# Kernel tuning notes

Hardware: AMD Instinct MI355X
Metric: run time of the kernel (lower is better)

## Reference

```python
import jax, jax.numpy as jnp
import numpy as np

TEMPERATURE = 1.0
NEG = -1e9
EPS = 1e-8


def setup_inputs() -> dict:
    key = jax.random.key(0)
    k1, k2, k3 = jax.random.split(key, 3)
    B, H = 524288, 32
    scores = jax.random.normal(k1, (B, H), dtype=jnp.float32)
    rankings = jax.random.randint(k2, (B, H), 0, 33, dtype=jnp.int32)
    mask = jax.random.randint(k3, (B, H), 0, 2, dtype=jnp.int32).astype(bool)
    return {"scores": scores, "rankings": rankings, "mask": mask}


def reference(scores, rankings, mask):
    B, H = scores.shape
    # effective validity: horse present AND has a ranking > 0 (top_k=None)
    m = mask & (rankings > 0)
    # masked, temperature-scaled scores; -1e9 entries underflow to exactly 0 in softmax
    s = jnp.where(m, scores / TEMPERATURE, NEG)
    p = jax.nn.softmax(s, axis=1)  # [B, H], ~0 at invalid slots

    n_valid = jnp.sum(m, axis=1)  # [B]
    # ideal order: valid horses sorted by ranking ascending (invalid pushed to end)
    rank_key = jnp.where(m, rankings, jnp.iinfo(jnp.int32).max)
    rank_order = jnp.argsort(rank_key, axis=1)          # stable sort
    # prediction order: valid horses in original index order (matches torch.where)
    pos_order = jnp.argsort(~m, axis=1)                 # stable: valid first

    q = jnp.take_along_axis(p, rank_order, axis=1)      # ideal_probs, aligned by list position
    pr = jnp.take_along_axis(p, pos_order, axis=1)      # pred_probs,  aligned by list position

    # positions >= n_valid are padding
    valid_pos = jnp.arange(H)[None, :] < n_valid[:, None]
    q_safe = jnp.where(valid_pos, q, 1.0)
    pr_safe = jnp.where(valid_pos, pr, 1.0)
    # KL(ideal || pred) with the original's log(pred + 1e-8)
    kl_terms = q_safe * (jnp.log(q_safe) - jnp.log(pr_safe + EPS))
    kl = jnp.sum(jnp.where(valid_pos, kl_terms, 0.0), axis=1)  # [B]

    # rows with <= 1 valid ranked horse are skipped entirely
    row_ok = n_valid > 1
    n_rows = jnp.maximum(jnp.sum(row_ok), 1)
    return jnp.sum(jnp.where(row_ok, kl, 0.0)) / n_rows  # reduction='mean'
```

## Files before the change

### kernel.cpp

```cpp
#include <hip/hip_runtime.h>
#include <stdint.h>


#define H 32
#define BLK 256
#define WPB 4
#define ROWD 17
#define WREGION (64 * ROWD)

typedef short s16x2 __attribute__((ext_vector_type(2)));
union PK { uint32_t u; s16x2 v; };

__global__ __launch_bounds__(BLK) void listwise_kernel(
    const float* __restrict__ scores,
    const int* __restrict__ rankings,
    const unsigned char* __restrict__ mask_u8,
    float* __restrict__ part_kl,
    float* __restrict__ part_cnt,
    int nrows)
{
    __shared__ uint32_t stage[WPB * WREGION];
    __shared__ float s_kl[WPB], s_cnt[WPB];

    const int tid  = threadIdx.x;
    const int lane = tid & 63;
    const int wid  = tid >> 6;
    uint32_t* wbuf = &stage[wid * WREGION];
    const int wrow0 = blockIdx.x * BLK + wid * 64;

    unsigned char probe = mask_u8[lane];
    const bool mask_is_i32 =
        (__ballot(((lane & 3) != 0) && (probe != 0)) == 0ull);

    float kl = 0.0f, cnt = 0.0f;

    uint32_t kp[16], sp[16];
    int nv = 0;
    bool have_row = false;
    unsigned short* rowp = (unsigned short*)&wbuf[lane * ROWD];

    if (wrow0 + 64 <= nrows) {
        have_row = true;

        const uint4* r4 = (const uint4*)(rankings + (size_t)wrow0 * H);
        if (mask_is_i32) {
            const uint4* m4 =
                (const uint4*)((const uint32_t*)mask_u8 + (size_t)wrow0 * H);
            #pragma unroll
            for (int c = 0; c < 8; ++c) {
                const uint4 rv = r4[lane + 64 * c];
                const uint4 mv = m4[lane + 64 * c];
                const int L = (lane + 64 * c) << 2;
                const uint32_t t0 = (mv.x != 0u && (int)rv.x > 0) ? (rv.x << 5) : 0x4000u;
                const uint32_t t1 = (mv.y != 0u && (int)rv.y > 0) ? (rv.y << 5) : 0x4000u;
                const uint32_t t2 = (mv.z != 0u && (int)rv.z > 0) ? (rv.z << 5) : 0x4000u;
                const uint32_t t3 = (mv.w != 0u && (int)rv.w > 0) ? (rv.w << 5) : 0x4000u;
                uint32_t* d = &wbuf[(L >> 5) * ROWD + ((L & 31) >> 1)];
                d[0] = t0 | (t1 << 16);
                d[1] = t2 | (t3 << 16);
            }
        } else {
            const uint32_t* m1 = (const uint32_t*)(mask_u8 + (size_t)wrow0 * H);
            #pragma unroll
            for (int c = 0; c < 8; ++c) {
                const uint4 rv = r4[lane + 64 * c];
                const uint32_t mv = m1[lane + 64 * c];
                const int L = (lane + 64 * c) << 2;
                const uint32_t t0 = ((mv & 0x000000FFu) != 0u && (int)rv.x > 0) ? (rv.x << 5) : 0x4000u;
                const uint32_t t1 = ((mv & 0x0000FF00u) != 0u && (int)rv.y > 0) ? (rv.y << 5) : 0x4000u;
                const uint32_t t2 = ((mv & 0x00FF0000u) != 0u && (int)rv.z > 0) ? (rv.z << 5) : 0x4000u;
                const uint32_t t3 = ((mv & 0xFF000000u) != 0u && (int)rv.w > 0) ? (rv.w << 5) : 0x4000u;
                uint32_t* d = &wbuf[(L >> 5) * ROWD + ((L & 31) >> 1)];
                d[0] = t0 | (t1 << 16);
                d[1] = t2 | (t3 << 16);
            }
        }
        {
            const uint32_t* rb = &wbuf[lane * ROWD];
            uint32_t inv2 = 0;
            #pragma unroll
            for (int a = 0; a < 16; ++a) {
                const uint32_t w = rb[a];
                kp[a] = w | ((uint32_t)(2 * a) | (((uint32_t)(2 * a + 1)) << 16));
                inv2 += (w >> 14) & 0x00010001u;
            }
            nv = 32 - (int)((inv2 & 0xFFFFu) + (inv2 >> 16));
        }

        {
            const uint4* g4 = (const uint4*)(scores + (size_t)wrow0 * H);
            #pragma unroll
            for (int c = 0; c < 8; ++c) {
                const uint4 v = g4[lane + 64 * c];
                const int L = (lane + 64 * c) << 2;
                const uint32_t b0 = (v.x + 0x8000u) >> 16;
                const uint32_t b1 = (v.y + 0x8000u) >> 16;
                const uint32_t b2 = (v.z + 0x8000u) >> 16;
                const uint32_t b3 = (v.w + 0x8000u) >> 16;
                uint32_t* d = &wbuf[(L >> 5) * ROWD + ((L & 31) >> 1)];
                d[0] = b0 | (b1 << 16);
                d[1] = b2 | (b3 << 16);
            }
            const uint32_t* rb = &wbuf[lane * ROWD];
            int jp = 0;
            #pragma unroll
            for (int a = 0; a < 16; ++a) {
                const uint32_t sw = rb[a];
                sp[a] = sw;
                const uint32_t kw = kp[a];
                const bool v0 = (kw & 0xFFFFu) < 0x4000u;
                const bool v1 = (kw >> 16) < 0x4000u;
                rowp[v0 ? jp : 33] = (unsigned short)(sw & 0xFFFFu);
                jp += v0 ? 1 : 0;
                rowp[v1 ? jp : 33] = (unsigned short)(sw >> 16);
                jp += v1 ? 1 : 0;
            }
        }
    } else if (wrow0 + lane < nrows) {
        have_row = true;
        const int row = wrow0 + lane;
        const int*   rptr = rankings + (size_t)row * H;
        const float* sptr = scores + (size_t)row * H;
        uint32_t vbits = 0;
        if (mask_is_i32) {
            const int* mp = (const int*)mask_u8 + (size_t)row * H;
            #pragma unroll
            for (int k = 0; k < H; ++k) vbits |= (mp[k] != 0 ? 1u : 0u) << k;
        } else {
            const unsigned char* mp = mask_u8 + (size_t)row * H;
            #pragma unroll
            for (int k = 0; k < H; ++k) vbits |= (mp[k] != 0 ? 1u : 0u) << k;
        }
        int jp = 0;
        #pragma unroll
        for (int a = 0; a < 16; ++a) {
            uint32_t kq[2], bq[2];
            #pragma unroll
            for (int q = 0; q < 2; ++q) {
                const int k = 2 * a + q;
                const int r = rptr[k];
                const bool valid = (((vbits >> k) & 1u) != 0u) && (r > 0);
                kq[q] = valid ? ((((uint32_t)r) << 5) | (uint32_t)k)
                              : (0x4000u | (uint32_t)k);
                nv += valid ? 1 : 0;
                bq[q] = (__float_as_uint(sptr[k]) + 0x8000u) >> 16;
                rowp[valid ? jp : 33] = (unsigned short)bq[q];
                jp += valid ? 1 : 0;
            }
            kp[a] = kq[0] | (kq[1] << 16);
            sp[a] = bq[0] | (bq[1] << 16);
        }
    }

    if (have_row) {
        float se = 0.0f, num = 0.0f;
        #pragma unroll
        for (int i = 0; i < H; ++i) {
            const uint32_t pw = kp[i / 2];
            const uint32_t k16 = (i & 1) ? (pw >> 16) : (pw & 0xFFFFu);
            PK b; b.u = (k16 << 16) | k16;
            PK acc; acc.u = 0;
            #pragma unroll
            for (int m = 0; m < 16; ++m) {
                PK pm; pm.u = kp[m];
                s16x2 d = pm.v - b.v;
                acc.v = acc.v - (d >> 15);
            }
            const int j = (int)acc.v.x + (int)acc.v.y;
            const float g = __uint_as_float(((uint32_t)rowp[j]) << 16);
            const uint32_t sw = sp[i / 2];
            const float s_i = __uint_as_float((i & 1) ? (sw & 0xFFFF0000u)
                                                      : (sw << 16));
            const bool valid = k16 < 0x4000u;
            float e = __expf(s_i);
            e = valid ? e : 0.0f;
            const float d2 = valid ? (s_i - g) : 0.0f;
            se += e;
            num = __builtin_fmaf(e, d2, num);
        }
        if (nv > 1) { kl = __fdividef(num, se); cnt = 1.0f; }
    }

    #pragma unroll
    for (int m = 32; m >= 1; m >>= 1) {
        kl  += __shfl_xor(kl, m);
        cnt += __shfl_xor(cnt, m);
    }
    if (lane == 0) { s_kl[wid] = kl; s_cnt[wid] = cnt; }
    __syncthreads();
    if (tid == 0) {
        part_kl[blockIdx.x]  = s_kl[0] + s_kl[1] + s_kl[2] + s_kl[3];
        part_cnt[blockIdx.x] = s_cnt[0] + s_cnt[1] + s_cnt[2] + s_cnt[3];
    }
}

__global__ __launch_bounds__(256) void finalize_kernel(
    const float* __restrict__ part_kl,
    const float* __restrict__ part_cnt,
    float* __restrict__ out, int nblk)
{
    float k = 0.0f, c = 0.0f;
    for (int i = threadIdx.x; i < nblk; i += 256) {
        k += part_kl[i];
        c += part_cnt[i];
    }
    #pragma unroll
    for (int m = 32; m >= 1; m >>= 1) {
        k += __shfl_xor(k, m);
        c += __shfl_xor(c, m);
    }
    __shared__ float sk[4], sc[4];
    const int wid = threadIdx.x >> 6;
    if ((threadIdx.x & 63) == 0) { sk[wid] = k; sc[wid] = c; }
    __syncthreads();
    if (threadIdx.x == 0) {
        float K = sk[0] + sk[1] + sk[2] + sk[3];
        float C = sc[0] + sc[1] + sc[2] + sc[3];
        if (C < 1.0f) C = 1.0f;
        out[0] = K / C;
    }
}

extern "C" void kernel_launch(void* const* d_in, const int* in_sizes, int n_in,
                              void* d_out, int out_size, void* d_ws, size_t ws_size,
                              hipStream_t stream) {
    const float* scores = (const float*)d_in[0];
    const int* rankings = (const int*)d_in[1];
    const unsigned char* mask = (const unsigned char*)d_in[2];
    float* out = (float*)d_out;

    const int total = in_sizes[0];
    const int nrows = total / H;
    const int blocks = (nrows + BLK - 1) / BLK;

    float* part_kl  = (float*)d_ws;
    float* part_cnt = (float*)d_ws + blocks;

    listwise_kernel<<<blocks, BLK, 0, stream>>>(
        scores, rankings, mask, part_kl, part_cnt, nrows);

    finalize_kernel<<<1, 256, 0, stream>>>(part_kl, part_cnt, out, blocks);
}
```

Before: 207.2 us.

## Process two 64-row tiles per wave with register prefetch of next tile

Each wave now handles two 64-row tiles. Rankings, scores and the byte mask for the first tile are loaded into registers up front, and the next tile's loads are issued while the current tile is staged through LDS, so memory latency overlaps with compute. The grid shrinks by half and launch bounds request 4 blocks per SIMD. This costs extra VGPRs for the prefetch buffers, which could cause spills or lower occupancy.

```diff
diff --git a/kernel.cpp b/kernel.cpp
--- a/kernel.cpp
+++ b/kernel.cpp
@@ -5,13 +5,14 @@
 #define H 32
 #define BLK 256
 #define WPB 4
+#define NT 2
 #define ROWD 17
 #define WREGION (64 * ROWD)
 
 typedef short s16x2 __attribute__((ext_vector_type(2)));
 union PK { uint32_t u; s16x2 v; };
 
-__global__ __launch_bounds__(BLK) void listwise_kernel(
+__global__ __launch_bounds__(BLK, 4) void listwise_kernel(
     const float* __restrict__ scores,
     const int* __restrict__ rankings,
     const unsigned char* __restrict__ mask_u8,
@@ -26,72 +27,105 @@
     const int lane = tid & 63;
     const int wid  = tid >> 6;
     uint32_t* wbuf = &stage[wid * WREGION];
-    const int wrow0 = blockIdx.x * BLK + wid * 64;
+    const int wave_g   = blockIdx.x * WPB + wid;
+    const int row_base = wave_g * (NT * 64);
+
+    uint4 pr[8], ps[8];
+    uint32_t pmw[8];
+    const bool t0_full = (row_base + 64 <= nrows);
+    if (t0_full) {
+        const uint4* r4 = (const uint4*)(rankings + (size_t)row_base * H);
+        const uint4* s4 = (const uint4*)(scores + (size_t)row_base * H);
+        #pragma unroll
+        for (int c = 0; c < 8; ++c) pr[c] = r4[lane + 64 * c];
+        #pragma unroll
+        for (int c = 0; c < 8; ++c) ps[c] = s4[lane + 64 * c];
+    }
 
     unsigned char probe = mask_u8[lane];
     const bool mask_is_i32 =
         (__ballot(((lane & 3) != 0) && (probe != 0)) == 0ull);
+    if (t0_full && !mask_is_i32) {
+        const uint32_t* m1 = (const uint32_t*)(mask_u8 + (size_t)row_base * H);
+        #pragma unroll
+        for (int c = 0; c < 8; ++c) pmw[c] = m1[lane + 64 * c];
+    }
 
     float kl = 0.0f, cnt = 0.0f;
-
-    uint32_t kp[16], sp[16];
-    int nv = 0;
-    bool have_row = false;
     unsigned short* rowp = (unsigned short*)&wbuf[lane * ROWD];
 
-    if (wrow0 + 64 <= nrows) {
-        have_row = true;
-
-        const uint4* r4 = (const uint4*)(rankings + (size_t)wrow0 * H);
-        if (mask_is_i32) {
-            const uint4* m4 =
-                (const uint4*)((const uint32_t*)mask_u8 + (size_t)wrow0 * H);
+    #pragma unroll
+    for (int t = 0; t < NT; ++t) {
+        const int wrow0 = row_base + t * 64;
+        uint32_t kp[16], sp[16];
+        int nv = 0;
+        bool have = false;
+
+        if (wrow0 + 64 <= nrows) {
+            have = true;
+
+            if (!mask_is_i32) {
+                #pragma unroll
+                for (int c = 0; c < 8; ++c) {
+                    const uint4 rv = pr[c];
+                    const uint32_t mv = pmw[c];
+                    const int L = (lane + 64 * c) << 2;
+                    const uint32_t t0 = ((mv & 0x000000FFu) != 0u && (int)rv.x > 0) ? (rv.x << 5) : 0x4000u;
+                    const uint32_t t1 = ((mv & 0x0000FF00u) != 0u && (int)rv.y > 0) ? (rv.y << 5) : 0x4000u;
+                    const uint32_t t2 = ((mv & 0x00FF0000u) != 0u && (int)rv.z > 0) ? (rv.z << 5) : 0x4000u;
+                    const uint32_t t3 = ((mv & 0xFF000000u) != 0u && (int)rv.w > 0) ? (rv.w << 5) : 0x4000u;
+                    uint32_t* d = &wbuf[(L >> 5) * ROWD + ((L & 31) >> 1)];
+                    d[0] = t0 | (t1 << 16);
+                    d[1] = t2 | (t3 << 16);
+                }
+            } else {
+                const uint4* m4 =
+                    (const uint4*)((const uint32_t*)mask_u8 + (size_t)wrow0 * H);
+                #pragma unroll
+                for (int c = 0; c < 8; ++c) {
+                    const uint4 rv = pr[c];
+                    const uint4 mv = m4[lane + 64 * c];
+                    const int L = (lane + 64 * c) << 2;
+                    const uint32_t t0 = (mv.x != 0u && (int)rv.x > 0) ? (rv.x << 5) : 0x4000u;
+                    const uint32_t t1 = (mv.y != 0u && (int)rv.y > 0) ? (rv.y << 5) : 0x4000u;
+                    const uint32_t t2 = (mv.z != 0u && (int)rv.z > 0) ? (rv.z << 5) : 0x4000u;
+                    const uint32_t t3 = (mv.w != 0u && (int)rv.w > 0) ? (rv.w << 5) : 0x4000u;
+                    uint32_t* d = &wbuf[(L >> 5) * ROWD + ((L & 31) >> 1)];
+                    d[0] = t0 | (t1 << 16);
+                    d[1] = t2 | (t3 << 16);
+                }
+            }
+
+            if (t + 1 < NT) {
+                const int nr0 = row_base + (t + 1) * 64;
+                if (nr0 + 64 <= nrows) {
+                    const uint4* r4n = (const uint4*)(rankings + (size_t)nr0 * H);
+                    #pragma unroll
+                    for (int c = 0; c < 8; ++c) pr[c] = r4n[lane + 64 * c];
+                    if (!mask_is_i32) {
+                        const uint32_t* m1n =
+                            (const uint32_t*)(mask_u8 + (size_t)nr0 * H);
+                        #pragma unroll
+                        for (int c = 0; c < 8; ++c) pmw[c] = m1n[lane + 64 * c];
+                    }
+                }
+            }
+
+            {
+                const uint32_t* rb = &wbuf[lane * ROWD];
+                uint32_t inv2 = 0;
+                #pragma unroll
+                for (int a = 0; a < 16; ++a) {
+                    const uint32_t w = rb[a];
+                    kp[a] = w | ((uint32_t)(2 * a) | (((uint32_t)(2 * a + 1)) << 16));
+                    inv2 += (w >> 14) & 0x00010001u;
+                }
+                nv = 32 - (int)((inv2 & 0xFFFFu) + (inv2 >> 16));
+            }
+
             #pragma unroll
             for (int c = 0; c < 8; ++c) {
-                const uint4 rv = r4[lane + 64 * c];
-                const uint4 mv = m4[lane + 64 * c];
-                const int L = (lane + 64 * c) << 2;
-                const uint32_t t0 = (mv.x != 0u && (int)rv.x > 0) ? (rv.x << 5) : 0x4000u;
-                const uint32_t t1 = (mv.y != 0u && (int)rv.y > 0) ? (rv.y << 5) : 0x4000u;
-                const uint32_t t2 = (mv.z != 0u && (int)rv.z > 0) ? (rv.z << 5) : 0x4000u;
-                const uint32_t t3 = (mv.w != 0u && (int)rv.w > 0) ? (rv.w << 5) : 0x4000u;
-                uint32_t* d = &wbuf[(L >> 5) * ROWD + ((L & 31) >> 1)];
-                d[0] = t0 | (t1 << 16);
-                d[1] = t2 | (t3 << 16);
-            }
-        } else {
-            const uint32_t* m1 = (const uint32_t*)(mask_u8 + (size_t)wrow0 * H);
-            #pragma unroll
-            for (int c = 0; c < 8; ++c) {
-                const uint4 rv = r4[lane + 64 * c];
-                const uint32_t mv = m1[lane + 64 * c];
-                const int L = (lane + 64 * c) << 2;
-                const uint32_t t0 = ((mv & 0x000000FFu) != 0u && (int)rv.x > 0) ? (rv.x << 5) : 0x4000u;
-                const uint32_t t1 = ((mv & 0x0000FF00u) != 0u && (int)rv.y > 0) ? (rv.y << 5) : 0x4000u;
-                const uint32_t t2 = ((mv & 0x00FF0000u) != 0u && (int)rv.z > 0) ? (rv.z << 5) : 0x4000u;
-                const uint32_t t3 = ((mv & 0xFF000000u) != 0u && (int)rv.w > 0) ? (rv.w << 5) : 0x4000u;
-                uint32_t* d = &wbuf[(L >> 5) * ROWD + ((L & 31) >> 1)];
-                d[0] = t0 | (t1 << 16);
-                d[1] = t2 | (t3 << 16);
-            }
-        }
-        {
-            const uint32_t* rb = &wbuf[lane * ROWD];
-            uint32_t inv2 = 0;
-            #pragma unroll
-            for (int a = 0; a < 16; ++a) {
-                const uint32_t w = rb[a];
-                kp[a] = w | ((uint32_t)(2 * a) | (((uint32_t)(2 * a + 1)) << 16));
-                inv2 += (w >> 14) & 0x00010001u;
-            }
-            nv = 32 - (int)((inv2 & 0xFFFFu) + (inv2 >> 16));
-        }
-
-        {
-            const uint4* g4 = (const uint4*)(scores + (size_t)wrow0 * H);
-            #pragma unroll
-            for (int c = 0; c < 8; ++c) {
-                const uint4 v = g4[lane + 64 * c];
+                const uint4 v = ps[c];
                 const int L = (lane + 64 * c) << 2;
                 const uint32_t b0 = (v.x + 0x8000u) >> 16;
                 const uint32_t b1 = (v.y + 0x8000u) >> 16;
@@ -101,84 +135,96 @@
                 d[0] = b0 | (b1 << 16);
                 d[1] = b2 | (b3 << 16);
             }
-            const uint32_t* rb = &wbuf[lane * ROWD];
+
+            if (t + 1 < NT) {
+                const int nr0 = row_base + (t + 1) * 64;
+                if (nr0 + 64 <= nrows) {
+                    const uint4* s4n = (const uint4*)(scores + (size_t)nr0 * H);
+                    #pragma unroll
+                    for (int c = 0; c < 8; ++c) ps[c] = s4n[lane + 64 * c];
+                }
+            }
+
+            {
+                const uint32_t* rb = &wbuf[lane * ROWD];
+                int jp = 0;
+                #pragma unroll
+                for (int a = 0; a < 16; ++a) {
+                    const uint32_t sw = rb[a];
+                    sp[a] = sw;
+                    const uint32_t kw = kp[a];
+                    const bool v0 = (kw & 0xFFFFu) < 0x4000u;
+                    const bool v1 = (kw >> 16) < 0x4000u;
+                    rowp[v0 ? jp : 33] = (unsigned short)(sw & 0xFFFFu);
+                    jp += v0 ? 1 : 0;
+                    rowp[v1 ? jp : 33] = (unsigned short)(sw >> 16);
+                    jp += v1 ? 1 : 0;
+                }
+            }
+        } else if (wrow0 + lane < nrows) {
+            have = true;
+            const int row = wrow0 + lane;
+            const int*   rptr = rankings + (size_t)row * H;
+            const float* sptr = scores + (size_t)row * H;
+            uint32_t vbits = 0;
+            if (mask_is_i32) {
+                const int* mp = (const int*)mask_u8 + (size_t)row * H;
+                #pragma unroll
+                for (int k = 0; k < H; ++k) vbits |= (mp[k] != 0 ? 1u : 0u) << k;
+            } else {
+                const unsigned char* mp = mask_u8 + (size_t)row * H;
+                #pragma unroll
+                for (int k = 0; k < H; ++k) vbits |= (mp[k] != 0 ? 1u : 0u) << k;
+            }
             int jp = 0;
             #pragma unroll
             for (int a = 0; a < 16; ++a) {
-                const uint32_t sw = rb[a];
-                sp[a] = sw;
-                const uint32_t kw = kp[a];
-                const bool v0 = (kw & 0xFFFFu) < 0x4000u;
-                const bool v1 = (kw >> 16) < 0x4000u;
-                rowp[v0 ? jp : 33] = (unsigned short)(sw & 0xFFFFu);
-                jp += v0 ? 1 : 0;
-                rowp[v1 ? jp : 33] = (unsigned short)(sw >> 16);
-                jp += v1 ? 1 : 0;
+                uint32_t kq[2], bq[2];
+                #pragma unroll
+                for (int q = 0; q < 2; ++q) {
+                    const int k = 2 * a + q;
+                    const int r = rptr[k];
+                    const bool valid = (((vbits >> k) & 1u) != 0u) && (r > 0);
+                    kq[q] = valid ? ((((uint32_t)r) << 5) | (uint32_t)k)
+                                  : (0x4000u | (uint32_t)k);
+                    nv += valid ? 1 : 0;
+                    bq[q] = (__float_as_uint(sptr[k]) + 0x8000u) >> 16;
+                    rowp[valid ? jp : 33] = (unsigned short)bq[q];
+                    jp += valid ? 1 : 0;
+                }
+                kp[a] = kq[0] | (kq[1] << 16);
+                sp[a] = bq[0] | (bq[1] << 16);
             }
         }
-    } else if (wrow0 + lane < nrows) {
-        have_row = true;
-        const int row = wrow0 + lane;
-        const int*   rptr = rankings + (size_t)row * H;
-        const float* sptr = scores + (size_t)row * H;
-        uint32_t vbits = 0;
-        if (mask_is_i32) {
-            const int* mp = (const int*)mask_u8 + (size_t)row * H;
+
+        if (have) {
+            float se = 0.0f, num = 0.0f;
             #pragma unroll
-            for (int k = 0; k < H; ++k) vbits |= (mp[k] != 0 ? 1u : 0u) << k;
-        } else {
-            const unsigned char* mp = mask_u8 + (size_t)row * H;
-            #pragma unroll
-            for (int k = 0; k < H; ++k) vbits |= (mp[k] != 0 ? 1u : 0u) << k;
+            for (int i = 0; i < H; ++i) {
+                const uint32_t pw = kp[i / 2];
+                const uint32_t k16 = (i & 1) ? (pw >> 16) : (pw & 0xFFFFu);
+                PK b; b.u = (k16 << 16) | k16;
+                PK acc; acc.u = 0;
+                #pragma unroll
+                for (int m = 0; m < 16; ++m) {
+                    PK pm_; pm_.u = kp[m];
+                    s16x2 d = pm_.v - b.v;
+                    acc.v = acc.v - (d >> 15);
+                }
+                const int j = (int)acc.v.x + (int)acc.v.y;
+                const float g = __uint_as_float(((uint32_t)rowp[j]) << 16);
+                const uint32_t sw = sp[i / 2];
+                const float s_i = __uint_as_float((i & 1) ? (sw & 0xFFFF0000u)
+                                                          : (sw << 16));
+                const bool valid = k16 < 0x4000u;
+                float e = __expf(s_i);
+                e = valid ? e : 0.0f;
+                const float d2 = valid ? (s_i - g) : 0.0f;
+                se += e;
+                num = __builtin_fmaf(e, d2, num);
+            }
+            if (nv > 1) { kl += __fdividef(num, se); cnt += 1.0f; }
         }
-        int jp = 0;
-        #pragma unroll
-        for (int a = 0; a < 16; ++a) {
-            uint32_t kq[2], bq[2];
-            #pragma unroll
-            for (int q = 0; q < 2; ++q) {
-                const int k = 2 * a + q;
-                const int r = rptr[k];
-                const bool valid = (((vbits >> k) & 1u) != 0u) && (r > 0);
-                kq[q] = valid ? ((((uint32_t)r) << 5) | (uint32_t)k)
-                              : (0x4000u | (uint32_t)k);
-                nv += valid ? 1 : 0;
-                bq[q] = (__float_as_uint(sptr[k]) + 0x8000u) >> 16;
-                rowp[valid ? jp : 33] = (unsigned short)bq[q];
-                jp += valid ? 1 : 0;
-            }
-            kp[a] = kq[0] | (kq[1] << 16);
-            sp[a] = bq[0] | (bq[1] << 16);
-        }
-    }
-
-    if (have_row) {
-        float se = 0.0f, num = 0.0f;
-        #pragma unroll
-        for (int i = 0; i < H; ++i) {
-            const uint32_t pw = kp[i / 2];
-            const uint32_t k16 = (i & 1) ? (pw >> 16) : (pw & 0xFFFFu);
-            PK b; b.u = (k16 << 16) | k16;
-            PK acc; acc.u = 0;
-            #pragma unroll
-            for (int m = 0; m < 16; ++m) {
-                PK pm; pm.u = kp[m];
-                s16x2 d = pm.v - b.v;
-                acc.v = acc.v - (d >> 15);
-            }
-            const int j = (int)acc.v.x + (int)acc.v.y;
-            const float g = __uint_as_float(((uint32_t)rowp[j]) << 16);
-            const uint32_t sw = sp[i / 2];
-            const float s_i = __uint_as_float((i & 1) ? (sw & 0xFFFF0000u)
-                                                      : (sw << 16));
-            const bool valid = k16 < 0x4000u;
-            float e = __expf(s_i);
-            e = valid ? e : 0.0f;
-            const float d2 = valid ? (s_i - g) : 0.0f;
-            se += e;
-            num = __builtin_fmaf(e, d2, num);
-        }
-        if (nv > 1) { kl = __fdividef(num, se); cnt = 1.0f; }
     }
 
     #pragma unroll
@@ -231,7 +277,8 @@
 
     const int total = in_sizes[0];
     const int nrows = total / H;
-    const int blocks = (nrows + BLK - 1) / BLK;
+    const int rows_per_block = WPB * NT * 64;
+    const int blocks = (nrows + rows_per_block - 1) / rows_per_block;
 
     float* part_kl  = (float*)d_ws;
     float* part_cnt = (float*)d_ws + blocks;
```

Measured after the change: 227.8 us. 10.0% more time.

## Replace per-element rank counting with bitonic sort and batch global loads upfront

Applied to the files above, without the earlier changes.

The O(H^2) packed-int16 rank computation is replaced by a 32-element register bitonic sort of (key, score) words. Each slot's score is then paired with the compacted score at the same position read from LDS. All rankings, scores and mask loads for full tiles are also issued before any LDS work so memory latency overlaps. The sort costs roughly 240 compare-exchanges per row and raises register pressure from the 8x uint4 prefetch buffers, which may lower occupancy.

```diff
diff --git a/kernel.cpp b/kernel.cpp
--- a/kernel.cpp
+++ b/kernel.cpp
@@ -7,9 +7,6 @@
 #define WPB 4
 #define ROWD 17
 #define WREGION (64 * ROWD)
-
-typedef short s16x2 __attribute__((ext_vector_type(2)));
-union PK { uint32_t u; s16x2 v; };
 
 __global__ __launch_bounds__(BLK) void listwise_kernel(
     const float* __restrict__ scores,
@@ -28,27 +25,69 @@
     uint32_t* wbuf = &stage[wid * WREGION];
     const int wrow0 = blockIdx.x * BLK + wid * 64;
 
+    float kl = 0.0f, cnt = 0.0f;
+    uint32_t kp[16], sw[16];
+    int nv = 0;
+    bool have_row = false;
+    unsigned short* rowp = (unsigned short*)&wbuf[lane * ROWD];
+
+    const bool full = (wrow0 + 64 <= nrows);
+
+    uint4 pr[8], ps[8];
+    uint32_t pmw[8];
+    if (full) {
+        const uint4* r4 = (const uint4*)(rankings + (size_t)wrow0 * H);
+        const uint4* s4 = (const uint4*)(scores + (size_t)wrow0 * H);
+        const uint32_t* m1 = (const uint32_t*)(mask_u8 + (size_t)wrow0 * H);
+        #pragma unroll
+        for (int c = 0; c < 8; ++c) pr[c] = r4[lane + 64 * c];
+        #pragma unroll
+        for (int c = 0; c < 8; ++c) ps[c] = s4[lane + 64 * c];
+        #pragma unroll
+        for (int c = 0; c < 8; ++c) pmw[c] = m1[lane + 64 * c];
+    }
+
     unsigned char probe = mask_u8[lane];
     const bool mask_is_i32 =
         (__ballot(((lane & 3) != 0) && (probe != 0)) == 0ull);
 
-    float kl = 0.0f, cnt = 0.0f;
-
-    uint32_t kp[16], sp[16];
-    int nv = 0;
-    bool have_row = false;
-    unsigned short* rowp = (unsigned short*)&wbuf[lane * ROWD];
-
-    if (wrow0 + 64 <= nrows) {
+    if (full) {
         have_row = true;
 
-        const uint4* r4 = (const uint4*)(rankings + (size_t)wrow0 * H);
-        if (mask_is_i32) {
+        #pragma unroll
+        for (int c = 0; c < 8; ++c) {
+            const uint4 v = ps[c];
+            const int L = (lane + 64 * c) << 2;
+            uint32_t* d = &wbuf[(L >> 5) * ROWD + ((L & 31) >> 1)];
+            d[0] = ((v.x + 0x8000u) >> 16) | (((v.y + 0x8000u) >> 16) << 16);
+            d[1] = ((v.z + 0x8000u) >> 16) | (((v.w + 0x8000u) >> 16) << 16);
+        }
+        {
+            const uint32_t* rb = &wbuf[lane * ROWD];
+            #pragma unroll
+            for (int a = 0; a < 16; ++a) sw[a] = rb[a];
+        }
+
+        if (!mask_is_i32) {
+            #pragma unroll
+            for (int c = 0; c < 8; ++c) {
+                const uint4 rv = pr[c];
+                const uint32_t mv = pmw[c];
+                const int L = (lane + 64 * c) << 2;
+                const uint32_t t0 = ((mv & 0x000000FFu) != 0u && (int)rv.x > 0) ? (rv.x << 5) : 0x4000u;
+                const uint32_t t1 = ((mv & 0x0000FF00u) != 0u && (int)rv.y > 0) ? (rv.y << 5) : 0x4000u;
+                const uint32_t t2 = ((mv & 0x00FF0000u) != 0u && (int)rv.z > 0) ? (rv.z << 5) : 0x4000u;
+                const uint32_t t3 = ((mv & 0xFF000000u) != 0u && (int)rv.w > 0) ? (rv.w << 5) : 0x4000u;
+                uint32_t* d = &wbuf[(L >> 5) * ROWD + ((L & 31) >> 1)];
+                d[0] = t0 | (t1 << 16);
+                d[1] = t2 | (t3 << 16);
+            }
+        } else {
             const uint4* m4 =
                 (const uint4*)((const uint32_t*)mask_u8 + (size_t)wrow0 * H);
             #pragma unroll
             for (int c = 0; c < 8; ++c) {
-                const uint4 rv = r4[lane + 64 * c];
+                const uint4 rv = pr[c];
                 const uint4 mv = m4[lane + 64 * c];
                 const int L = (lane + 64 * c) << 2;
                 const uint32_t t0 = (mv.x != 0u && (int)rv.x > 0) ? (rv.x << 5) : 0x4000u;
@@ -59,21 +98,6 @@
                 d[0] = t0 | (t1 << 16);
                 d[1] = t2 | (t3 << 16);
             }
-        } else {
-            const uint32_t* m1 = (const uint32_t*)(mask_u8 + (size_t)wrow0 * H);
-            #pragma unroll
-            for (int c = 0; c < 8; ++c) {
-                const uint4 rv = r4[lane + 64 * c];
-                const uint32_t mv = m1[lane + 64 * c];
-                const int L = (lane + 64 * c) << 2;
-                const uint32_t t0 = ((mv & 0x000000FFu) != 0u && (int)rv.x > 0) ? (rv.x << 5) : 0x4000u;
-                const uint32_t t1 = ((mv & 0x0000FF00u) != 0u && (int)rv.y > 0) ? (rv.y << 5) : 0x4000u;
-                const uint32_t t2 = ((mv & 0x00FF0000u) != 0u && (int)rv.z > 0) ? (rv.z << 5) : 0x4000u;
-                const uint32_t t3 = ((mv & 0xFF000000u) != 0u && (int)rv.w > 0) ? (rv.w << 5) : 0x4000u;
-                uint32_t* d = &wbuf[(L >> 5) * ROWD + ((L & 31) >> 1)];
-                d[0] = t0 | (t1 << 16);
-                d[1] = t2 | (t3 << 16);
-            }
         }
         {
             const uint32_t* rb = &wbuf[lane * ROWD];
@@ -86,33 +110,17 @@
             }
             nv = 32 - (int)((inv2 & 0xFFFFu) + (inv2 >> 16));
         }
-
         {
-            const uint4* g4 = (const uint4*)(scores + (size_t)wrow0 * H);
-            #pragma unroll
-            for (int c = 0; c < 8; ++c) {
-                const uint4 v = g4[lane + 64 * c];
-                const int L = (lane + 64 * c) << 2;
-                const uint32_t b0 = (v.x + 0x8000u) >> 16;
-                const uint32_t b1 = (v.y + 0x8000u) >> 16;
-                const uint32_t b2 = (v.z + 0x8000u) >> 16;
-                const uint32_t b3 = (v.w + 0x8000u) >> 16;
-                uint32_t* d = &wbuf[(L >> 5) * ROWD + ((L & 31) >> 1)];
-                d[0] = b0 | (b1 << 16);
-                d[1] = b2 | (b3 << 16);
-            }
-            const uint32_t* rb = &wbuf[lane * ROWD];
             int jp = 0;
             #pragma unroll
             for (int a = 0; a < 16; ++a) {
-                const uint32_t sw = rb[a];
-                sp[a] = sw;
+                const uint32_t s2 = sw[a];
                 const uint32_t kw = kp[a];
                 const bool v0 = (kw & 0xFFFFu) < 0x4000u;
                 const bool v1 = (kw >> 16) < 0x4000u;
-                rowp[v0 ? jp : 33] = (unsigned short)(sw & 0xFFFFu);
+                rowp[v0 ? jp : 33] = (unsigned short)(s2 & 0xFFFFu);
                 jp += v0 ? 1 : 0;
-                rowp[v1 ? jp : 33] = (unsigned short)(sw >> 16);
+                rowp[v1 ? jp : 33] = (unsigned short)(s2 >> 16);
                 jp += v1 ? 1 : 0;
             }
         }
@@ -148,35 +156,55 @@
                 jp += valid ? 1 : 0;
             }
             kp[a] = kq[0] | (kq[1] << 16);
-            sp[a] = bq[0] | (bq[1] << 16);
+            sw[a] = bq[0] | (bq[1] << 16);
         }
     }
 
     if (have_row) {
+        uint32_t w32[32];
+        #pragma unroll
+        for (int a = 0; a < 16; ++a) {
+            const uint32_t kw = kp[a], s2 = sw[a];
+            w32[2 * a]     = (kw << 16) | (s2 & 0xFFFFu);
+            w32[2 * a + 1] = (kw & 0xFFFF0000u) | (s2 >> 16);
+        }
+        #pragma unroll
+        for (int k = 2; k <= 32; k <<= 1) {
+            #pragma unroll
+            for (int j = k >> 1; j > 0; j >>= 1) {
+                #pragma unroll
+                for (int i = 0; i < 32; ++i) {
+                    const int l = i ^ j;
+                    if (l > i) {
+                        const uint32_t a = w32[i], b = w32[l];
+                        const uint32_t mn = a < b ? a : b;
+                        const uint32_t mx = a < b ? b : a;
+                        const bool up = ((i & k) == 0);
+                        w32[i] = up ? mn : mx;
+                        w32[l] = up ? mx : mn;
+                    }
+                }
+            }
+        }
+
         float se = 0.0f, num = 0.0f;
-        #pragma unroll
-        for (int i = 0; i < H; ++i) {
-            const uint32_t pw = kp[i / 2];
-            const uint32_t k16 = (i & 1) ? (pw >> 16) : (pw & 0xFFFFu);
-            PK b; b.u = (k16 << 16) | k16;
-            PK acc; acc.u = 0;
-            #pragma unroll
-            for (int m = 0; m < 16; ++m) {
-                PK pm; pm.u = kp[m];
-                s16x2 d = pm.v - b.v;
-                acc.v = acc.v - (d >> 15);
-            }
-            const int j = (int)acc.v.x + (int)acc.v.y;
-            const float g = __uint_as_float(((uint32_t)rowp[j]) << 16);
-            const uint32_t sw = sp[i / 2];
-            const float s_i = __uint_as_float((i & 1) ? (sw & 0xFFFF0000u)
-                                                      : (sw << 16));
-            const bool valid = k16 < 0x4000u;
-            float e = __expf(s_i);
-            e = valid ? e : 0.0f;
-            const float d2 = valid ? (s_i - g) : 0.0f;
-            se += e;
-            num = __builtin_fmaf(e, d2, num);
+        const uint32_t* rbd = &wbuf[lane * ROWD];
+        #pragma unroll
+        for (int a = 0; a < 16; ++a) {
+            const uint32_t cw = rbd[a];
+            #pragma unroll
+            for (int q = 0; q < 2; ++q) {
+                const uint32_t wv = w32[2 * a + q];
+                const bool valid = wv < 0x40000000u;
+                const float s_i = __uint_as_float(wv << 16);
+                const uint32_t c16 = q ? (cw >> 16) : (cw & 0xFFFFu);
+                const float g = __uint_as_float(c16 << 16);
+                float e = __expf(s_i);
+                e = valid ? e : 0.0f;
+                const float d2 = valid ? (s_i - g) : 0.0f;
+                se += e;
+                num = __builtin_fmaf(e, d2, num);
+            }
         }
         if (nv > 1) { kl = __fdividef(num, se); cnt = 1.0f; }
     }
```

Measured after the change: 199.7 us. 3.6% less time.

## Map rows to lanes with wave-level bitonic sort and ballot compaction

Applied to the files above, without the earlier changes.

Replaces the per-thread row processing, which used LDS staging and quadratic rank counting, with a scheme where each wave handles two rows per step and each lane holds one element. Ranking order comes from a shuffle-based bitonic sort, and valid scores are compacted with ballot/mbcnt plus ds_permute. The softmax-weighted KL terms are then reduced with cross-lane shuffles. The grid becomes a fixed 2048 blocks that loop over row pairs, prefetching the next pair into registers. This drops the LDS traffic and O(H^2) compute, at the cost of narrow 4-byte loads and a serial per-wave loop.

```diff
diff --git a/kernel.cpp b/kernel.cpp
--- a/kernel.cpp
+++ b/kernel.cpp
@@ -5,11 +5,6 @@
 #define H 32
 #define BLK 256
 #define WPB 4
-#define ROWD 17
-#define WREGION (64 * ROWD)
-
-typedef short s16x2 __attribute__((ext_vector_type(2)));
-union PK { uint32_t u; s16x2 v; };
 
 __global__ __launch_bounds__(BLK) void listwise_kernel(
     const float* __restrict__ scores,
@@ -17,176 +12,103 @@
     const unsigned char* __restrict__ mask_u8,
     float* __restrict__ part_kl,
     float* __restrict__ part_cnt,
-    int nrows)
+    int nrows, int ipw)
 {
-    __shared__ uint32_t stage[WPB * WREGION];
     __shared__ float s_kl[WPB], s_cnt[WPB];
 
     const int tid  = threadIdx.x;
     const int lane = tid & 63;
     const int wid  = tid >> 6;
-    uint32_t* wbuf = &stage[wid * WREGION];
-    const int wrow0 = blockIdx.x * BLK + wid * 64;
+    const int e5   = lane & 31;
+    const int h    = lane >> 5;
+
+    const long long wave_g = (long long)blockIdx.x * WPB + wid;
+    const long long tpairs = ((long long)nrows + 1) >> 1;
+    const long long pbase  = wave_g * ipw;
+    const long long pend   = (pbase + ipw < tpairs) ? (pbase + ipw) : tpairs;
 
     unsigned char probe = mask_u8[lane];
     const bool mask_is_i32 =
         (__ballot(((lane & 3) != 0) && (probe != 0)) == 0ull);
 
-    float kl = 0.0f, cnt = 0.0f;
+    float kl_acc = 0.0f, cnt_acc = 0.0f;
 
-    uint32_t kp[16], sp[16];
-    int nv = 0;
-    bool have_row = false;
-    unsigned short* rowp = (unsigned short*)&wbuf[lane * ROWD];
+    if (pbase < pend) {
+        const size_t maxidx = (size_t)nrows * H - 1;
 
-    if (wrow0 + 64 <= nrows) {
-        have_row = true;
+        size_t b = (size_t)pbase * 64 + lane;
+        if (b > maxidx) b = maxidx;
+        int      rv = rankings[b];
+        float    sv = scores[b];
+        uint32_t mv = mask_is_i32 ? (uint32_t)((const int*)mask_u8)[b]
+                                  : (uint32_t)mask_u8[b];
 
-        const uint4* r4 = (const uint4*)(rankings + (size_t)wrow0 * H);
-        if (mask_is_i32) {
-            const uint4* m4 =
-                (const uint4*)((const uint32_t*)mask_u8 + (size_t)wrow0 * H);
+        for (long long p = pbase; p < pend; ++p) {
+            const long long pn = (p + 1 < pend) ? (p + 1) : p;
+            size_t bn = (size_t)pn * 64 + lane;
+            if (bn > maxidx) bn = maxidx;
+            const int      rvn = rankings[bn];
+            const float    svn = scores[bn];
+            const uint32_t mvn = mask_is_i32
+                ? (uint32_t)((const int*)mask_u8)[bn]
+                : (uint32_t)mask_u8[bn];
+
+            const int  row   = (int)(2 * p) + h;
+            const bool valid = (row < nrows) && (mv != 0u) && (rv > 0);
+            const uint32_t b16 = (__float_as_uint(sv) + 0x8000u) >> 16;
+            const uint32_t key = valid ? (((uint32_t)rv << 5) | (uint32_t)e5)
+                                       : (0x4000u | (uint32_t)e5);
+            uint32_t w = (key << 16) | b16;
+            const float gsrc = __uint_as_float(b16 << 16);
+
+            const unsigned long long vm = __ballot(valid);
+            const uint32_t mb = __builtin_amdgcn_mbcnt_hi(
+                (uint32_t)(vm >> 32),
+                __builtin_amdgcn_mbcnt_lo((uint32_t)vm, 0u));
+            const int plo = __builtin_popcountll(vm & 0xffffffffull);
+            const int phi = __builtin_popcountll(vm >> 32);
+            const int q   = (int)mb - (h ? plo : 0);
+            const int nvh = h ? phi : plo;
+            const int slot = (valid ? q : (nvh + (e5 - q))) + (h << 5);
+            const float gq = __uint_as_float(
+                __builtin_amdgcn_ds_permute(slot << 2, (int)__float_as_uint(gsrc)));
+
             #pragma unroll
-            for (int c = 0; c < 8; ++c) {
-                const uint4 rv = r4[lane + 64 * c];
-                const uint4 mv = m4[lane + 64 * c];
-                const int L = (lane + 64 * c) << 2;
-                const uint32_t t0 = (mv.x != 0u && (int)rv.x > 0) ? (rv.x << 5) : 0x4000u;
-                const uint32_t t1 = (mv.y != 0u && (int)rv.y > 0) ? (rv.y << 5) : 0x4000u;
-                const uint32_t t2 = (mv.z != 0u && (int)rv.z > 0) ? (rv.z << 5) : 0x4000u;
-                const uint32_t t3 = (mv.w != 0u && (int)rv.w > 0) ? (rv.w << 5) : 0x4000u;
-                uint32_t* d = &wbuf[(L >> 5) * ROWD + ((L & 31) >> 1)];
-                d[0] = t0 | (t1 << 16);
-                d[1] = t2 | (t3 << 16);
+            for (int k = 2; k <= 32; k <<= 1) {
+                #pragma unroll
+                for (int j = k >> 1; j > 0; j >>= 1) {
+                    const uint32_t pw = (uint32_t)__shfl_xor((int)w, j);
+                    const uint32_t mn = w < pw ? w : pw;
+                    const uint32_t mx = w < pw ? pw : w;
+                    const bool tm = (((e5 & j) == 0) != ((e5 & k) == 0));
+                    w = tm ? mx : mn;
+                }
             }
-        } else {
-            const uint32_t* m1 = (const uint32_t*)(mask_u8 + (size_t)wrow0 * H);
+
+            const bool  vld = (w < 0x40000000u);
+            const float sb  = __uint_as_float(w << 16);
+            float e = __expf(sb);
+            e = vld ? e : 0.0f;
+            const float d = vld ? (sb - gq) : 0.0f;
+            float se = e;
+            float nm = e * d;
             #pragma unroll
-            for (int c = 0; c < 8; ++c) {
-                const uint4 rv = r4[lane + 64 * c];
-                const uint32_t mv = m1[lane + 64 * c];
-                const int L = (lane + 64 * c) << 2;
-                const uint32_t t0 = ((mv & 0x000000FFu) != 0u && (int)rv.x > 0) ? (rv.x << 5) : 0x4000u;
-                const uint32_t t1 = ((mv & 0x0000FF00u) != 0u && (int)rv.y > 0) ? (rv.y << 5) : 0x4000u;
-                const uint32_t t2 = ((mv & 0x00FF0000u) != 0u && (int)rv.z > 0) ? (rv.z << 5) : 0x4000u;
-                const uint32_t t3 = ((mv & 0xFF000000u) != 0u && (int)rv.w > 0) ? (rv.w << 5) : 0x4000u;
-                uint32_t* d = &wbuf[(L >> 5) * ROWD + ((L & 31) >> 1)];
-                d[0] = t0 | (t1 << 16);
-                d[1] = t2 | (t3 << 16);
+            for (int j2 = 1; j2 <= 16; j2 <<= 1) {
+                se += __shfl_xor(se, j2);
+                nm += __shfl_xor(nm, j2);
             }
-        }
-        {
-            const uint32_t* rb = &wbuf[lane * ROWD];
-            uint32_t inv2 = 0;
-            #pragma unroll
-            for (int a = 0; a < 16; ++a) {
-                const uint32_t w = rb[a];
-                kp[a] = w | ((uint32_t)(2 * a) | (((uint32_t)(2 * a + 1)) << 16));
-                inv2 += (w >> 14) & 0x00010001u;
-            }
-            nv = 32 - (int)((inv2 & 0xFFFFu) + (inv2 >> 16));
-        }
+            const bool rok = (nvh > 1);
+            const float contrib = rok ? __fdividef(nm, se) : 0.0f;
+            kl_acc  += (e5 == 0) ? contrib : 0.0f;
+            cnt_acc += (e5 == 0 && rok) ? 1.0f : 0.0f;
 
-        {
-            const uint4* g4 = (const uint4*)(scores + (size_t)wrow0 * H);
-            #pragma unroll
-            for (int c = 0; c < 8; ++c) {
-                const uint4 v = g4[lane + 64 * c];
-                const int L = (lane + 64 * c) << 2;
-                const uint32_t b0 = (v.x + 0x8000u) >> 16;
-                const uint32_t b1 = (v.y + 0x8000u) >> 16;
-                const uint32_t b2 = (v.z + 0x8000u) >> 16;
-                const uint32_t b3 = (v.w + 0x8000u) >> 16;
-                uint32_t* d = &wbuf[(L >> 5) * ROWD + ((L & 31) >> 1)];
-                d[0] = b0 | (b1 << 16);
-                d[1] = b2 | (b3 << 16);
-            }
-            const uint32_t* rb = &wbuf[lane * ROWD];
-            int jp = 0;
-            #pragma unroll
-            for (int a = 0; a < 16; ++a) {
-                const uint32_t sw = rb[a];
-                sp[a] = sw;
-                const uint32_t kw = kp[a];
-                const bool v0 = (kw & 0xFFFFu) < 0x4000u;
-                const bool v1 = (kw >> 16) < 0x4000u;
-                rowp[v0 ? jp : 33] = (unsigned short)(sw & 0xFFFFu);
-                jp += v0 ? 1 : 0;
-                rowp[v1 ? jp : 33] = (unsigned short)(sw >> 16);
-                jp += v1 ? 1 : 0;
-            }
-        }
-    } else if (wrow0 + lane < nrows) {
-        have_row = true;
-        const int row = wrow0 + lane;
-        const int*   rptr = rankings + (size_t)row * H;
-        const float* sptr = scores + (size_t)row * H;
-        uint32_t vbits = 0;
-        if (mask_is_i32) {
-            const int* mp = (const int*)mask_u8 + (size_t)row * H;
-            #pragma unroll
-            for (int k = 0; k < H; ++k) vbits |= (mp[k] != 0 ? 1u : 0u) << k;
-        } else {
-            const unsigned char* mp = mask_u8 + (size_t)row * H;
-            #pragma unroll
-            for (int k = 0; k < H; ++k) vbits |= (mp[k] != 0 ? 1u : 0u) << k;
-        }
-        int jp = 0;
-        #pragma unroll
-        for (int a = 0; a < 16; ++a) {
-            uint32_t kq[2], bq[2];
-            #pragma unroll
-            for (int q = 0; q < 2; ++q) {
-                const int k = 2 * a + q;
-                const int r = rptr[k];
-                const bool valid = (((vbits >> k) & 1u) != 0u) && (r > 0);
-                kq[q] = valid ? ((((uint32_t)r) << 5) | (uint32_t)k)
-                              : (0x4000u | (uint32_t)k);
-                nv += valid ? 1 : 0;
-                bq[q] = (__float_as_uint(sptr[k]) + 0x8000u) >> 16;
-                rowp[valid ? jp : 33] = (unsigned short)bq[q];
-                jp += valid ? 1 : 0;
-            }
-            kp[a] = kq[0] | (kq[1] << 16);
-            sp[a] = bq[0] | (bq[1] << 16);
+            rv = rvn; sv = svn; mv = mvn;
         }
     }
 
-    if (have_row) {
-        float se = 0.0f, num = 0.0f;
-        #pragma unroll
-        for (int i = 0; i < H; ++i) {
-            const uint32_t pw = kp[i / 2];
-            const uint32_t k16 = (i & 1) ? (pw >> 16) : (pw & 0xFFFFu);
-            PK b; b.u = (k16 << 16) | k16;
-            PK acc; acc.u = 0;
-            #pragma unroll
-            for (int m = 0; m < 16; ++m) {
-                PK pm; pm.u = kp[m];
-                s16x2 d = pm.v - b.v;
-                acc.v = acc.v - (d >> 15);
-            }
-            const int j = (int)acc.v.x + (int)acc.v.y;
-            const float g = __uint_as_float(((uint32_t)rowp[j]) << 16);
-            const uint32_t sw = sp[i / 2];
-            const float s_i = __uint_as_float((i & 1) ? (sw & 0xFFFF0000u)
-                                                      : (sw << 16));
-            const bool valid = k16 < 0x4000u;
-            float e = __expf(s_i);
-            e = valid ? e : 0.0f;
-            const float d2 = valid ? (s_i - g) : 0.0f;
-            se += e;
-            num = __builtin_fmaf(e, d2, num);
-        }
-        if (nv > 1) { kl = __fdividef(num, se); cnt = 1.0f; }
-    }
-
-    #pragma unroll
-    for (int m = 32; m >= 1; m >>= 1) {
-        kl  += __shfl_xor(kl, m);
-        cnt += __shfl_xor(cnt, m);
-    }
-    if (lane == 0) { s_kl[wid] = kl; s_cnt[wid] = cnt; }
+    kl_acc  += __shfl_xor(kl_acc, 32);
+    cnt_acc += __shfl_xor(cnt_acc, 32);
+    if (lane == 0) { s_kl[wid] = kl_acc; s_cnt[wid] = cnt_acc; }
     __syncthreads();
     if (tid == 0) {
         part_kl[blockIdx.x]  = s_kl[0] + s_kl[1] + s_kl[2] + s_kl[3];
@@ -231,13 +153,17 @@
 
     const int total = in_sizes[0];
     const int nrows = total / H;
-    const int blocks = (nrows + BLK - 1) / BLK;
+    const int blocks = 2048;
+    const long long tpairs = ((long long)nrows + 1) >> 1;
+    const long long waves = (long long)blocks * WPB;
+    int ipw = (int)((tpairs + waves - 1) / waves);
+    if (ipw < 1) ipw = 1;
 
     float* part_kl  = (float*)d_ws;
     float* part_cnt = (float*)d_ws + blocks;
 
     listwise_kernel<<<blocks, BLK, 0, stream>>>(
-        scores, rankings, mask, part_kl, part_cnt, nrows);
+        scores, rankings, mask, part_kl, part_cnt, nrows, ipw);
 
     finalize_kernel<<<1, 256, 0, stream>>>(part_kl, part_cnt, out, blocks);
 }
```

After: 215.9 us. +4.2%, slower.
